# Kernel tuning notes

Measured on AMD Instinct MI355X. Metric: run time of the kernel, lower is better.

## Reference

```python
import jax, jax.numpy as jnp
import numpy as np

# Fixed-step Dormand-Prince RK45 (dopri5) over t in [0, 1].
# torchdiffeq's dopri5 is adaptive; an adaptive while-loop is not
# reverse-differentiable in JAX, so we use the same dopri5 tableau with a
# fixed step count, which reproduces the per-step math exactly.
N_STEPS = 64

# dopri5 Butcher tableau (a-matrix rows; b = 5th-order weights = row a7)
A21 = 1/5
A31, A32 = 3/40, 9/40
A41, A42, A43 = 44/45, -56/15, 32/9
A51, A52, A53, A54 = 19372/6561, -25360/2187, 64448/6561, -212/729
A61, A62, A63, A64, A65 = 9017/3168, -355/33, 46732/5247, 49/176, -5103/18656
B1, B3, B4, B5, B6 = 35/384, 500/1113, 125/192, -2187/6784, 11/84


def setup_inputs() -> dict:
    key = jax.random.key(0)
    ks = jax.random.split(key, 7)
    data_dim, hidden_dim, batch = 512, 1024, 4096
    s1 = 1.0 / np.sqrt(data_dim)
    s2 = 1.0 / np.sqrt(hidden_dim)
    return {
        "x":  jax.random.normal(ks[0], (batch, data_dim), jnp.float32),
        "W1": jax.random.normal(ks[1], (hidden_dim, data_dim), jnp.float32) * s1,
        "b1": jax.random.normal(ks[2], (hidden_dim,), jnp.float32) * s1,
        "W2": jax.random.normal(ks[3], (hidden_dim, hidden_dim), jnp.float32) * s2,
        "b2": jax.random.normal(ks[4], (hidden_dim,), jnp.float32) * s2,
        "W3": jax.random.normal(ks[5], (data_dim, hidden_dim), jnp.float32) * s2,
        "b3": jax.random.normal(ks[6], (data_dim,), jnp.float32) * s2,
    }


def reference(x, W1, b1, W2, b2, W3, b3):
    def f(y):  # ODEFunc MLP: fc1 -> relu -> fc2 -> relu -> fc3 (autonomous)
        h = jax.nn.relu(y @ W1.T + b1)
        h = jax.nn.relu(h @ W2.T + b2)
        return h @ W3.T + b3

    h = jnp.float32(1.0 / N_STEPS)

    def step(y, _):
        k1 = f(y)
        k2 = f(y + h * (A21 * k1))
        k3 = f(y + h * (A31 * k1 + A32 * k2))
        k4 = f(y + h * (A41 * k1 + A42 * k2 + A43 * k3))
        k5 = f(y + h * (A51 * k1 + A52 * k2 + A53 * k3 + A54 * k4))
        k6 = f(y + h * (A61 * k1 + A62 * k2 + A63 * k3 + A64 * k4 + A65 * k5))
        y_next = y + h * (B1 * k1 + B3 * k3 + B4 * k4 + B5 * k5 + B6 * k6)
        return y_next, None

    y_final, _ = jax.lax.scan(step, x, None, length=N_STEPS)
    return y_final
```

## Files before the change

kernel.cpp:

```cpp
#include <hip/hip_runtime.h>
#include <hip/hip_bf16.h>
#include <stdint.h>
#include <stddef.h>

using bf16_t = __hip_bfloat16;
typedef __attribute__((ext_vector_type(8))) short short8;
typedef __attribute__((ext_vector_type(4))) float f32x4;

__device__ __forceinline__ void gload_lds16(void* lds, const void* g) {
  __builtin_amdgcn_global_load_lds(
      (const __attribute__((address_space(1))) unsigned int*)g,
      (__attribute__((address_space(3))) unsigned int*)lds,
      16, 0, 0);
}

template<int MFRAG, bool RELU, bool COMBINE, bool STORE_K, bool STORE_YF>
__global__ __launch_bounds__(256, 2)
void gemm_bt(const bf16_t* __restrict__ A, const bf16_t* __restrict__ B,
             const float* __restrict__ bias,
             bf16_t* __restrict__ obf,
             bf16_t* __restrict__ kout,
             float* __restrict__ yf_out,
             const float* __restrict__ y_in,
             const bf16_t* __restrict__ kp0, const bf16_t* __restrict__ kp1,
             const bf16_t* __restrict__ kp2, const bf16_t* __restrict__ kp3,
             float c0, float c1, float c2, float c3, float ccur,
             int M, int N, int K, int lgx)
{
  constexpr int BM = 32 * MFRAG;
  constexpr int BN = 64;
  constexpr int NFRAG = 2;
  constexpr int AR = BM / 32;
  constexpr int BR = 2;
  constexpr int LPT = AR + BR;

  __shared__ __align__(16) bf16_t As[3][BM * 64];
  __shared__ __align__(16) bf16_t Bs[3][BN * 64];

  const int t    = threadIdx.x;
  const int lane = t & 63;
  const int wid  = t >> 6;
  const int wm   = wid >> 1;
  const int wn   = wid & 1;

  const int nwg = gridDim.x, bid = blockIdx.x;
  const int swz = (bid & 7) * (nwg >> 3) + (bid >> 3);
  const int gxm = (1 << lgx) - 1;
  const int bx  = swz & gxm;
  const int by  = swz >> lgx;
  const int bn0 = bx * BN, bm0 = by * BM;

  const bf16_t* Ag = A + (size_t)bm0 * K;
  const bf16_t* Bg = B + (size_t)bn0 * K;

  f32x4 acc[MFRAG][NFRAG] = {};

  auto stage = [&](int b, int kt) {
    const int k0 = kt * 64;
#pragma unroll
    for (int r = 0; r < AR; ++r) {
      int ch  = t + r * 256;
      int row = ch >> 3, s = ch & 7;
      int sl  = s ^ (row & 7);
      gload_lds16(&As[b][ch * 8], Ag + (size_t)row * K + k0 + sl * 8);
    }
#pragma unroll
    for (int r = 0; r < BR; ++r) {
      int ch  = t + r * 256;
      int row = ch >> 3, s = ch & 7;
      int sl  = s ^ (row & 7);
      gload_lds16(&Bs[b][ch * 8], Bg + (size_t)row * K + k0 + sl * 8);
    }
  };

  const int nt = K >> 6;
  stage(0, 0);
  stage(1, 1);

  const int ro = lane & 15;
  const int ks = lane >> 4;

  int c = 0;
  for (int tt = 0; tt < nt; ++tt) {
    if (tt == nt - 1) {
      asm volatile("s_waitcnt vmcnt(0)" ::: "memory");
    } else if constexpr (LPT == 6) {
      asm volatile("s_waitcnt vmcnt(6)" ::: "memory");
    } else {
      asm volatile("s_waitcnt vmcnt(4)" ::: "memory");
    }
    __builtin_amdgcn_s_barrier();
    asm volatile("" ::: "memory");

    if (tt + 2 < nt) {
      int nb = c + 2; if (nb >= 3) nb -= 3;
      stage(nb, tt + 2);
    }

#pragma unroll
    for (int kk = 0; kk < 2; ++kk) {
      short8 af[MFRAG], bfr[NFRAG];
      const int slot = kk * 4 + ks;
#pragma unroll
      for (int mi = 0; mi < MFRAG; ++mi) {
        int row = wm * (MFRAG * 16) + mi * 16 + ro;
        int ch  = row * 8 + (slot ^ (row & 7));
        af[mi]  = *(const short8*)&As[c][ch * 8];
      }
#pragma unroll
      for (int ni = 0; ni < NFRAG; ++ni) {
        int row = wn * 32 + ni * 16 + ro;
        int ch  = row * 8 + (slot ^ (row & 7));
        bfr[ni] = *(const short8*)&Bs[c][ch * 8];
      }
      __builtin_amdgcn_s_setprio(1);
#pragma unroll
      for (int mi = 0; mi < MFRAG; ++mi)
#pragma unroll
        for (int ni = 0; ni < NFRAG; ++ni)
          acc[mi][ni] = __builtin_amdgcn_mfma_f32_16x16x32_bf16(
              af[mi], bfr[ni], acc[mi][ni], 0, 0, 0);
      __builtin_amdgcn_s_setprio(0);
    }

    if (++c == 3) c = 0;
  }

  const int rb = bm0 + wm * (MFRAG * 16);
  const int cb = bn0 + wn * 32;
#pragma unroll
  for (int mi = 0; mi < MFRAG; ++mi) {
#pragma unroll
    for (int ni = 0; ni < NFRAG; ++ni) {
      const int col = cb + ni * 16 + ro;
      const float bv = bias[col];
#pragma unroll
      for (int r = 0; r < 4; ++r) {
        const int row = rb + mi * 16 + (lane >> 4) * 4 + r;
        const size_t idx = (size_t)row * N + col;
        float v = acc[mi][ni][r] + bv;
        if (RELU) v = fmaxf(v, 0.f);
        if (COMBINE) {
          if (STORE_K) kout[idx] = __float2bfloat16(v);
          float z = y_in[idx] + ccur * v;
          if (kp0) z += c0 * __bfloat162float(kp0[idx]);
          if (kp1) z += c1 * __bfloat162float(kp1[idx]);
          if (kp2) z += c2 * __bfloat162float(kp2[idx]);
          if (kp3) z += c3 * __bfloat162float(kp3[idx]);
          if (STORE_YF) yf_out[idx] = z;
          obf[idx] = __float2bfloat16(z);
        } else {
          obf[idx] = __float2bfloat16(v);
        }
      }
    }
  }
}

__global__ void init_y_kernel(const float* __restrict__ x, float* __restrict__ y,
                              bf16_t* __restrict__ yb, int n) {
  int i = blockIdx.x * blockDim.x + threadIdx.x;
  if (i < n) {
    float v = x[i];
    y[i]  = v;
    yb[i] = __float2bfloat16(v);
  }
}

__global__ void f2b_kernel(const float* __restrict__ in, bf16_t* __restrict__ out, int n) {
  int i = blockIdx.x * blockDim.x + threadIdx.x;
  if (i < n) out[i] = __float2bfloat16(in[i]);
}

extern "C" void kernel_launch(void* const* d_in, const int* in_sizes, int n_in,
                              void* d_out, int out_size, void* d_ws, size_t ws_size,
                              hipStream_t stream)
{
  const float* x  = (const float*)d_in[0];
  const float* W1 = (const float*)d_in[1];
  const float* b1 = (const float*)d_in[2];
  const float* W2 = (const float*)d_in[3];
  const float* b2 = (const float*)d_in[4];
  const float* W3 = (const float*)d_in[5];
  const float* b3 = (const float*)d_in[6];

  const int data   = in_sizes[6];
  const int hidden = in_sizes[2];
  const int batch  = in_sizes[0] / data;

  char* ws = (char*)d_ws;
  size_t off = 0;
  auto alloc = [&](size_t bytes) -> void* {
    off = (off + 255) & ~(size_t)255;
    void* p = ws + off;
    off += bytes;
    return p;
  };
  const size_t nyd = (size_t)batch * data;
  const size_t nh  = (size_t)batch * hidden;

  float*  y   = (float*)alloc(nyd * 4);
  bf16_t* yb  = (bf16_t*)alloc(nyd * 2);
  bf16_t* zb  = (bf16_t*)alloc(nyd * 2);
  bf16_t* h1  = (bf16_t*)alloc(nh * 2);
  bf16_t* h2  = (bf16_t*)alloc(nh * 2);
  bf16_t* k1  = (bf16_t*)alloc(nyd * 2);
  bf16_t* k2  = (bf16_t*)alloc(nyd * 2);
  bf16_t* k3  = (bf16_t*)alloc(nyd * 2);
  bf16_t* k4  = (bf16_t*)alloc(nyd * 2);
  bf16_t* k5  = (bf16_t*)alloc(nyd * 2);
  bf16_t* W1b = (bf16_t*)alloc((size_t)hidden * data * 2);
  bf16_t* W2b = (bf16_t*)alloc((size_t)hidden * hidden * 2);
  bf16_t* W3b = (bf16_t*)alloc((size_t)data * hidden * 2);

  {
    int n = (int)nyd;
    init_y_kernel<<<(n + 255) / 256, 256, 0, stream>>>(x, y, yb, n);
    n = hidden * data;
    f2b_kernel<<<(n + 255) / 256, 256, 0, stream>>>(W1, W1b, n);
    n = hidden * hidden;
    f2b_kernel<<<(n + 255) / 256, 256, 0, stream>>>(W2, W2b, n);
    n = data * hidden;
    f2b_kernel<<<(n + 255) / 256, 256, 0, stream>>>(W3, W3b, n);
  }

  const double hh = 1.0 / 64.0;
  const float hA21 = (float)(hh * (1.0/5.0));
  const float hA31 = (float)(hh * (3.0/40.0)),    hA32 = (float)(hh * (9.0/40.0));
  const float hA41 = (float)(hh * (44.0/45.0)),   hA42 = (float)(hh * (-56.0/15.0)),
              hA43 = (float)(hh * (32.0/9.0));
  const float hA51 = (float)(hh * (19372.0/6561.0)),  hA52 = (float)(hh * (-25360.0/2187.0)),
              hA53 = (float)(hh * (64448.0/6561.0)),  hA54 = (float)(hh * (-212.0/729.0));
  const float hA61 = (float)(hh * (9017.0/3168.0)),   hA62 = (float)(hh * (-355.0/33.0)),
              hA63 = (float)(hh * (46732.0/5247.0)),  hA64 = (float)(hh * (49.0/176.0)),
              hA65 = (float)(hh * (-5103.0/18656.0));
  const float hB1 = (float)(hh * (35.0/384.0)),   hB3 = (float)(hh * (500.0/1113.0)),
              hB4 = (float)(hh * (125.0/192.0)),  hB5 = (float)(hh * (-2187.0/6784.0)),
              hB6 = (float)(hh * (11.0/84.0));

  const dim3 blk(256);
  const int gridH = (hidden / 64) * (batch / 128);
  const int grid3 = (data / 64) * (batch / 64);
  const int lgxH = 4, lgx3 = 3;

  auto mlp_front = [&](const bf16_t* zin) {
    gemm_bt<4, true, false, false, false><<<gridH, blk, 0, stream>>>(
        zin, W1b, b1, h1, nullptr, nullptr, nullptr,
        nullptr, nullptr, nullptr, nullptr, 0.f, 0.f, 0.f, 0.f, 0.f,
        batch, hidden, data, lgxH);
    gemm_bt<4, true, false, false, false><<<gridH, blk, 0, stream>>>(
        h1, W2b, b2, h2, nullptr, nullptr, nullptr,
        nullptr, nullptr, nullptr, nullptr, 0.f, 0.f, 0.f, 0.f, 0.f,
        batch, hidden, hidden, lgxH);
  };

  auto stage_k = [&](bf16_t* kout, const bf16_t* p0, float cc0, const bf16_t* p1, float cc1,
                     const bf16_t* p2, float cc2, const bf16_t* p3, float cc3, float ccur) {
    gemm_bt<2, false, true, true, false><<<grid3, blk, 0, stream>>>(
        h2, W3b, b3, zb, kout, nullptr, y,
        p0, p1, p2, p3, cc0, cc1, cc2, cc3, ccur,
        batch, data, hidden, lgx3);
  };

  for (int step = 0; step < 64; ++step) {
    mlp_front(yb);
    stage_k(k1, nullptr, 0.f, nullptr, 0.f, nullptr, 0.f, nullptr, 0.f, hA21);
    mlp_front(zb);
    stage_k(k2, k1, hA31, nullptr, 0.f, nullptr, 0.f, nullptr, 0.f, hA32);
    mlp_front(zb);
    stage_k(k3, k1, hA41, k2, hA42, nullptr, 0.f, nullptr, 0.f, hA43);
    mlp_front(zb);
    stage_k(k4, k1, hA51, k2, hA52, k3, hA53, nullptr, 0.f, hA54);
    mlp_front(zb);
    stage_k(k5, k1, hA61, k2, hA62, k3, hA63, k4, hA64, hA65);
    mlp_front(zb);
    float* yf = (step == 63) ? (float*)d_out : y;
    gemm_bt<2, false, true, false, true><<<grid3, blk, 0, stream>>>(
        h2, W3b, b3, yb, nullptr, yf, y,
        k1, k3, k4, k5, hB1, hB3, hB4, hB5, hB6,
        batch, data, hidden, lgx3);
  }
}
```

Measured before the change: 18.72 ms.

## Use uniform 64x64 tiles with double buffering and higher occupancy

Drops the MFRAG template so every GEMM, including the hidden-layer ones that used 128x64 tiles, now uses 64x64 tiles. The LDS ring shrinks from three buffers to two and the loop waits on vmcnt(0) every iteration. Launch bounds rise from 2 to 4 waves per SIMD to get more resident blocks per CU and smaller buffers. In exchange the hidden GEMMs get less data reuse per tile, and prefetch depth drops to one stage, which risks exposing global-load latency.

Measured after the change: 18.26 ms. -2.4%, faster.

```diff
diff --git a/kernel.cpp b/kernel.cpp
--- a/kernel.cpp
+++ b/kernel.cpp
@@ -14,8 +14,8 @@
       16, 0, 0);
 }
 
-template<int MFRAG, bool RELU, bool COMBINE, bool STORE_K, bool STORE_YF>
-__global__ __launch_bounds__(256, 2)
+template<bool RELU, bool COMBINE, bool STORE_K, bool STORE_YF>
+__global__ __launch_bounds__(256, 4)
 void gemm_bt(const bf16_t* __restrict__ A, const bf16_t* __restrict__ B,
              const float* __restrict__ bias,
              bf16_t* __restrict__ obf,
@@ -27,15 +27,8 @@
              float c0, float c1, float c2, float c3, float ccur,
              int M, int N, int K, int lgx)
 {
-  constexpr int BM = 32 * MFRAG;
-  constexpr int BN = 64;
-  constexpr int NFRAG = 2;
-  constexpr int AR = BM / 32;
-  constexpr int BR = 2;
-  constexpr int LPT = AR + BR;
-
-  __shared__ __align__(16) bf16_t As[3][BM * 64];
-  __shared__ __align__(16) bf16_t Bs[3][BN * 64];
+  __shared__ __align__(16) bf16_t As[2][64 * 64];
+  __shared__ __align__(16) bf16_t Bs[2][64 * 64];
 
   const int t    = threadIdx.x;
   const int lane = t & 63;
@@ -48,24 +41,24 @@
   const int gxm = (1 << lgx) - 1;
   const int bx  = swz & gxm;
   const int by  = swz >> lgx;
-  const int bn0 = bx * BN, bm0 = by * BM;
+  const int bn0 = bx * 64, bm0 = by * 64;
 
   const bf16_t* Ag = A + (size_t)bm0 * K;
   const bf16_t* Bg = B + (size_t)bn0 * K;
 
-  f32x4 acc[MFRAG][NFRAG] = {};
+  f32x4 acc[2][2] = {};
 
   auto stage = [&](int b, int kt) {
     const int k0 = kt * 64;
 #pragma unroll
-    for (int r = 0; r < AR; ++r) {
+    for (int r = 0; r < 2; ++r) {
       int ch  = t + r * 256;
       int row = ch >> 3, s = ch & 7;
       int sl  = s ^ (row & 7);
       gload_lds16(&As[b][ch * 8], Ag + (size_t)row * K + k0 + sl * 8);
     }
 #pragma unroll
-    for (int r = 0; r < BR; ++r) {
+    for (int r = 0; r < 2; ++r) {
       int ch  = t + r * 256;
       int row = ch >> 3, s = ch & 7;
       int sl  = s ^ (row & 7);
@@ -75,63 +68,51 @@
 
   const int nt = K >> 6;
   stage(0, 0);
-  stage(1, 1);
 
   const int ro = lane & 15;
   const int ks = lane >> 4;
 
-  int c = 0;
   for (int tt = 0; tt < nt; ++tt) {
-    if (tt == nt - 1) {
-      asm volatile("s_waitcnt vmcnt(0)" ::: "memory");
-    } else if constexpr (LPT == 6) {
-      asm volatile("s_waitcnt vmcnt(6)" ::: "memory");
-    } else {
-      asm volatile("s_waitcnt vmcnt(4)" ::: "memory");
-    }
+    const int c = tt & 1;
+    asm volatile("s_waitcnt vmcnt(0)" ::: "memory");
     __builtin_amdgcn_s_barrier();
     asm volatile("" ::: "memory");
 
-    if (tt + 2 < nt) {
-      int nb = c + 2; if (nb >= 3) nb -= 3;
-      stage(nb, tt + 2);
-    }
+    if (tt + 1 < nt) stage(c ^ 1, tt + 1);
 
 #pragma unroll
     for (int kk = 0; kk < 2; ++kk) {
-      short8 af[MFRAG], bfr[NFRAG];
+      short8 af[2], bfr[2];
       const int slot = kk * 4 + ks;
 #pragma unroll
-      for (int mi = 0; mi < MFRAG; ++mi) {
-        int row = wm * (MFRAG * 16) + mi * 16 + ro;
+      for (int mi = 0; mi < 2; ++mi) {
+        int row = wm * 32 + mi * 16 + ro;
         int ch  = row * 8 + (slot ^ (row & 7));
         af[mi]  = *(const short8*)&As[c][ch * 8];
       }
 #pragma unroll
-      for (int ni = 0; ni < NFRAG; ++ni) {
+      for (int ni = 0; ni < 2; ++ni) {
         int row = wn * 32 + ni * 16 + ro;
         int ch  = row * 8 + (slot ^ (row & 7));
         bfr[ni] = *(const short8*)&Bs[c][ch * 8];
       }
       __builtin_amdgcn_s_setprio(1);
 #pragma unroll
-      for (int mi = 0; mi < MFRAG; ++mi)
-#pragma unroll
-        for (int ni = 0; ni < NFRAG; ++ni)
+      for (int mi = 0; mi < 2; ++mi)
+#pragma unroll
+        for (int ni = 0; ni < 2; ++ni)
           acc[mi][ni] = __builtin_amdgcn_mfma_f32_16x16x32_bf16(
               af[mi], bfr[ni], acc[mi][ni], 0, 0, 0);
       __builtin_amdgcn_s_setprio(0);
     }
-
-    if (++c == 3) c = 0;
-  }
-
-  const int rb = bm0 + wm * (MFRAG * 16);
+  }
+
+  const int rb = bm0 + wm * 32;
   const int cb = bn0 + wn * 32;
 #pragma unroll
-  for (int mi = 0; mi < MFRAG; ++mi) {
-#pragma unroll
-    for (int ni = 0; ni < NFRAG; ++ni) {
+  for (int mi = 0; mi < 2; ++mi) {
+#pragma unroll
+    for (int ni = 0; ni < 2; ++ni) {
       const int col = cb + ni * 16 + ro;
       const float bv = bias[col];
 #pragma unroll
@@ -239,16 +220,16 @@
               hB6 = (float)(hh * (11.0/84.0));
 
   const dim3 blk(256);
-  const int gridH = (hidden / 64) * (batch / 128);
+  const int gridH = (hidden / 64) * (batch / 64);
   const int grid3 = (data / 64) * (batch / 64);
   const int lgxH = 4, lgx3 = 3;
 
   auto mlp_front = [&](const bf16_t* zin) {
-    gemm_bt<4, true, false, false, false><<<gridH, blk, 0, stream>>>(
+    gemm_bt<true, false, false, false><<<gridH, blk, 0, stream>>>(
         zin, W1b, b1, h1, nullptr, nullptr, nullptr,
         nullptr, nullptr, nullptr, nullptr, 0.f, 0.f, 0.f, 0.f, 0.f,
         batch, hidden, data, lgxH);
-    gemm_bt<4, true, false, false, false><<<gridH, blk, 0, stream>>>(
+    gemm_bt<true, false, false, false><<<gridH, blk, 0, stream>>>(
         h1, W2b, b2, h2, nullptr, nullptr, nullptr,
         nullptr, nullptr, nullptr, nullptr, 0.f, 0.f, 0.f, 0.f, 0.f,
         batch, hidden, hidden, lgxH);
@@ -256,7 +237,7 @@
 
   auto stage_k = [&](bf16_t* kout, const bf16_t* p0, float cc0, const bf16_t* p1, float cc1,
                      const bf16_t* p2, float cc2, const bf16_t* p3, float cc3, float ccur) {
-    gemm_bt<2, false, true, true, false><<<grid3, blk, 0, stream>>>(
+    gemm_bt<false, true, true, false><<<grid3, blk, 0, stream>>>(
         h2, W3b, b3, zb, kout, nullptr, y,
         p0, p1, p2, p3, cc0, cc1, cc2, cc3, ccur,
         batch, data, hidden, lgx3);
@@ -275,7 +256,7 @@
     stage_k(k5, k1, hA61, k2, hA62, k3, hA63, k4, hA64, hA65);
     mlp_front(zb);
     float* yf = (step == 63) ? (float*)d_out : y;
-    gemm_bt<2, false, true, false, true><<<grid3, blk, 0, stream>>>(
+    gemm_bt<false, true, false, true><<<grid3, blk, 0, stream>>>(
         h2, W3b, b3, yb, nullptr, yf, y,
         k1, k3, k4, k5, hB1, hB3, hB4, hB5, hB6,
         batch, data, hidden, lgx3);
```
